# Optimization experiments

Measured on AMD Instinct MI355X. Metric: run time of the kernel, lower is better.

## Reference

```python
import jax, jax.numpy as jnp
import numpy as np

H = 256  # hidden_size
C = 512  # in_channels


def _gru_dir(x, w_ih, w_hh, b_ih, b_hh, reverse):
    # x: (B, T, Cin); w_ih: (3H, Cin); w_hh: (3H, H); gate order r,z,n (PyTorch)
    if reverse:
        x = x[:, ::-1, :]
    xp = jnp.einsum('btc,gc->btg', x, w_ih) + b_ih  # (B, T, 3H), batched GEMM
    h0 = jnp.zeros((x.shape[0], w_hh.shape[1]), x.dtype)

    def step(h, xp_t):  # xp_t: (B, 3H)
        gh = h @ w_hh.T + b_hh
        xr, xz, xn = jnp.split(xp_t, 3, axis=-1)
        hr, hz, hn = jnp.split(gh, 3, axis=-1)
        r = jax.nn.sigmoid(xr + hr)
        z = jax.nn.sigmoid(xz + hz)
        n = jnp.tanh(xn + r * hn)
        h_new = (1.0 - z) * n + z * h
        return h_new, h_new

    _, ys = jax.lax.scan(step, h0, jnp.swapaxes(xp, 0, 1))  # (T, B, H)
    ys = jnp.swapaxes(ys, 0, 1)  # (B, T, H)
    if reverse:
        ys = ys[:, ::-1, :]
    return ys


def _bigru_layer(x, wf, whf, bf, bhf, wr, whr, br, bhr):
    fwd = _gru_dir(x, wf, whf, bf, bhf, reverse=False)
    bwd = _gru_dir(x, wr, whr, br, bhr, reverse=True)
    return jnp.concatenate([fwd, bwd], axis=-1)  # (B, T, 2H)


def setup_inputs() -> dict:
    key = jax.random.key(0)
    ks = jax.random.split(key, 17)
    k = 1.0 / np.sqrt(H)  # PyTorch default init bound
    u = lambda kk, shp: jax.random.uniform(kk, shp, jnp.float32, -k, k)
    x = jax.random.normal(ks[0], (64, 512, 512, 1), jnp.float32)
    inp = {'x': x}
    # layer 0: input size C; layer 1: input size 2H
    sizes = {'l0': C, 'l1': 2 * H}
    i = 1
    for layer in ('l0', 'l1'):
        cin = sizes[layer]
        for d in ('f', 'r'):
            inp[f'w_ih_{layer}{d}'] = u(ks[i], (3 * H, cin)); i += 1
            inp[f'w_hh_{layer}{d}'] = u(ks[i], (3 * H, H)); i += 1
            inp[f'b_ih_{layer}{d}'] = u(ks[i], (3 * H,)); i += 1
            inp[f'b_hh_{layer}{d}'] = u(ks[i], (3 * H,)); i += 1
    return inp


def reference(x, w_ih_l0f, w_hh_l0f, b_ih_l0f, b_hh_l0f,
              w_ih_l0r, w_hh_l0r, b_ih_l0r, b_hh_l0r,
              w_ih_l1f, w_hh_l1f, b_ih_l1f, b_hh_l1f,
              w_ih_l1r, w_hh_l1r, b_ih_l1r, b_hh_l1r):
    b, c, w, h = x.shape
    seq = x.reshape(b, c, w * h).transpose(0, 2, 1)  # (B, T, C)
    y0 = _bigru_layer(seq, w_ih_l0f, w_hh_l0f, b_ih_l0f, b_hh_l0f,
                      w_ih_l0r, w_hh_l0r, b_ih_l0r, b_hh_l0r)
    y1 = _bigru_layer(y0, w_ih_l1f, w_hh_l1f, b_ih_l1f, b_hh_l1f,
                      w_ih_l1r, w_hh_l1r, b_ih_l1r, b_hh_l1r)
    return y1  # (B, T, 2H)
```

## Files before the change

### kernel.cpp

```cpp
#include <hip/hip_runtime.h>


typedef unsigned short u16;
typedef unsigned char u8;
typedef __attribute__((ext_vector_type(8))) short short8;
typedef __attribute__((ext_vector_type(4))) float f32x4;
typedef __attribute__((ext_vector_type(4))) int i32x4;

#define C1 (-1.4426950408889634f)
#define C2 (-2.8853900817779268f)
#define QS 258064.0f
#define C1S (C1 / QS)
#define C2S (C2 / QS)
#define MAGIC 12582912.0f

static __device__ __forceinline__ u16 f2bf(float x){
  union { float f; unsigned u; } v; v.f = x;
  unsigned r = v.u + 0x7fffu + ((v.u >> 16) & 1u);
  return (u16)(r >> 16);
}
static __device__ __forceinline__ float bf2f(u16 b){
  union { float f; unsigned u; } v; v.u = ((unsigned)b) << 16;
  return v.f;
}
static __device__ __forceinline__ unsigned cvt_pk_bf16(float lo, float hi){
  unsigned d;
  asm("v_cvt_pk_bf16_f32 %0, %1, %2" : "=v"(d) : "v"(lo), "v"(hi));
  return d;
}
static __device__ __forceinline__ unsigned q8(float x, float scale){
  union { float f; unsigned u; } v; v.f = fmaf(x, scale, MAGIC);
  return v.u & 0xffu;
}
#if __has_builtin(__builtin_amdgcn_exp2f)
#define EXP2(x) __builtin_amdgcn_exp2f(x)
#else
#define EXP2(x) exp2f(x)
#endif
#define RCP(x) __builtin_amdgcn_rcpf(x)

#define TT 512
#define BB 64
#define HH 256
#define GG 768
#define CC 512

#define HLB 320

__global__ __launch_bounds__(256) void k_transpose(const float* __restrict__ x,
                                                   u16* __restrict__ xT)
{
  __shared__ u16 tile[32][33];
  const int b  = blockIdx.z;
  const int c0 = blockIdx.y * 32, t0 = blockIdx.x * 32;
  const int tx = threadIdx.x & 31, ty = threadIdx.x >> 5;
  const float* xb = x + (size_t)b * CC * TT;
  #pragma unroll
  for (int i = 0; i < 4; ++i){
    int c = c0 + ty + i * 8;
    tile[ty + i * 8][tx] = f2bf(xb[(size_t)c * TT + t0 + tx]);
  }
  __syncthreads();
  const int bb2 = b >> 1, mrow = b & 1;
  #pragma unroll
  for (int i = 0; i < 4; ++i){
    int t = t0 + ty + i * 8;
    size_t rowp = ((size_t)bb2 * TT + t) * 2 + mrow;
    xT[rowp * CC + c0 + tx] = tile[tx][ty + i * 8];
  }
}

__global__ __launch_bounds__(256) void k_gemm(const u16* __restrict__ A,
    const float* __restrict__ wf, const float* __restrict__ wr,
    const float* __restrict__ bif, const float* __restrict__ bir,
    const float* __restrict__ bhf, const float* __restrict__ bhr,
    u16* __restrict__ xpA, u16* __restrict__ xpB)
{
  __shared__ u16 As[64][72];
  __shared__ u16 Bs[64][72];
  const int tid = threadIdx.x;
  const int n0  = blockIdx.x * 64;
  const int m0  = blockIdx.y * 64;
  const int dir = (n0 >= GG) ? 1 : 0;
  const int gb  = n0 - dir * GG;
  const float* W  = dir ? wr : wf;
  const float* BI = dir ? bir : bif;
  const float* BH = dir ? bhr : bhf;

  const int w = tid >> 6, l = tid & 63, q = l >> 4, r = l & 15;
  f32x4 acc[4] = {};

  for (int k0 = 0; k0 < CC; k0 += 64){
    #pragma unroll
    for (int i = 0; i < 2; ++i){
      int ch = tid + 256 * i;
      int row = ch >> 3, c8 = ch & 7;
      *(uint4*)&As[row][c8 * 8] =
          *(const uint4*)&A[(size_t)(m0 + row) * CC + k0 + c8 * 8];
    }
    #pragma unroll
    for (int i = 0; i < 4; ++i){
      int ch = tid + 256 * i;
      int row = ch >> 4, c4 = ch & 15;
      const float* s = &W[(size_t)(gb + row) * CC + k0 + c4 * 4];
      float4 fv = *(const float4*)s;
      unsigned p0 = (unsigned)f2bf(fv.x) | ((unsigned)f2bf(fv.y) << 16);
      unsigned p1 = (unsigned)f2bf(fv.z) | ((unsigned)f2bf(fv.w) << 16);
      *(uint2*)&Bs[row][c4 * 4] = make_uint2(p0, p1);
    }
    __syncthreads();
    #pragma unroll
    for (int kk = 0; kk < 2; ++kk){
      short8 a = *(const short8*)&As[w * 16 + r][kk * 32 + q * 8];
      #pragma unroll
      for (int nt = 0; nt < 4; ++nt){
        short8 b = *(const short8*)&Bs[nt * 16 + r][kk * 32 + q * 8];
        acc[nt] = __builtin_amdgcn_mfma_f32_16x16x32_bf16(a, b, acc[nt], 0, 0, 0);
      }
    }
    __syncthreads();
  }
  #pragma unroll
  for (int nt = 0; nt < 4; ++nt){
    const int g  = gb + nt * 16 + r;
    const int gi = g >> 8;
    const int c  = g & 255;
    const int wvl = c >> 5, cw = c & 31;
    const int ct = cw >> 4, rp = cw & 15;
    const float bias = (gi < 2) ? (BI[g] + BH[g]) : BI[g];
    const float sc   = (gi < 2) ? C1 : C2;
    #pragma unroll
    for (int j = 0; j < 4; ++j){
      const int row  = m0 + w * 16 + q * 4 + j;
      const int t    = (row >> 1) & 511;
      const int bb2  = row >> 10;
      const int mrow = row & 1;
      const int lane = wvl * 64 + (ct * 2 + mrow) * 16 + rp;
      const size_t base = ((size_t)(dir * 32 + bb2) * TT + t) * 512 + lane;
      const u16 v = f2bf(sc * (acc[nt][j] + bias));
      if (gi < 2) xpA[base * 2 + gi] = v;
      else        xpB[base]          = v;
    }
  }
}

template<int OUT_F32>
__global__ __launch_bounds__(512, 2) void k_rec(
    const u16* __restrict__ xpA, const u16* __restrict__ xpB,
    const float* __restrict__ whf, const float* __restrict__ whr,
    const float* __restrict__ bhf, const float* __restrict__ bhr,
    void* __restrict__ yout)
{
  __shared__ __align__(16) u8 hl[2][2][HLB];
  const int tid = threadIdx.x;
  const int d = blockIdx.x >> 5, bb2 = blockIdx.x & 31;
  const int wv = tid >> 6, l = tid & 63, q = l >> 4, r = l & 15;
  const int upper = (l >= 32);
  const int rodd  = q & 1;
  const int rl = l & 1;
  const float* WH = d ? whr : whf;
  const float* BH = d ? bhr : bhf;

  i32x4 Bf[3][2][4];
  #pragma unroll
  for (int gi = 0; gi < 3; ++gi)
    #pragma unroll
    for (int ct = 0; ct < 2; ++ct){
      int g = gi * HH + wv * 32 + ct * 16 + r;
      #pragma unroll
      for (int kk = 0; kk < 4; ++kk){
        const float* s = &WH[(size_t)g * HH + kk * 64 + q * 16];
        i32x4 bfv;
        #pragma unroll
        for (int c4 = 0; c4 < 4; ++c4){
          float4 fv = *(const float4*)(s + c4 * 4);
          unsigned b0 = q8(fv.x, 2032.0f);
          unsigned b1 = q8(fv.y, 2032.0f);
          unsigned b2 = q8(fv.z, 2032.0f);
          unsigned b3 = q8(fv.w, 2032.0f);
          bfv[c4] = (int)(b0 | (b1 << 8) | (b2 << 16) | (b3 << 24));
        }
        Bf[gi][ct][kk] = bfv;
      }
    }

  const int col = wv * 32 + (upper ? 16 : 0) + r;
  const float bnl = C2 * BH[2 * HH + col];
  float ho = 0.0f;

  for (int i = tid; i < 2 * 2 * HLB; i += 512) ((u8*)hl)[i] = 0;

  const int t0 = d ? (TT - 1) : 0;
  const int dstep = d ? -1 : 1;

  const size_t blk = (size_t)(d * 32 + bb2) * TT;
  const u16* pxA = xpA + ((blk + t0) * 512 + tid) * 2;
  const u16* pxB = xpB + ((blk + t0) * 512 + tid);
  const ptrdiff_t pxAs = (ptrdiff_t)dstep * 512 * 2;
  const ptrdiff_t pxBs = (ptrdiff_t)dstep * 512;

  struct XP { unsigned a; u16 b; };
  XP cxA, cxB;
  cxA.a = *(const unsigned*)pxA;  cxA.b = *pxB;
  pxA += pxAs; pxB += pxBs;

  u16*   py = nullptr;  float* pf = nullptr;
  if (OUT_F32){
    float* yf = (float*)yout;
    pf = yf + (((size_t)(bb2 * 2 + rodd) * TT + t0) * (2 * HH)) + (size_t)d * HH + col;
  } else {
    u16* yb = (u16*)yout;
    py = yb + (((size_t)bb2 * TT + t0) * 2 + rodd) * 512 + (size_t)d * HH + col;
  }
  const ptrdiff_t pys = (ptrdiff_t)dstep * 2 * 512;
  const ptrdiff_t pfs = (ptrdiff_t)dstep * 2 * HH;

  __syncthreads();

  auto step = [&](int s, int cur, XP* cxu, XP* cxl) {
    const int nxt = cur ^ 1;
    cxl->a = *(const unsigned*)pxA;
    cxl->b = *pxB;
    if (s < TT - 2){ pxA += pxAs; pxB += pxBs; }

    i32x4 acc[3][2] = {};
    #pragma unroll
    for (int kk = 0; kk < 4; ++kk){
      i32x4 af = *(const i32x4*)&hl[cur][rl][kk * 64 + q * 16];
      #pragma unroll
      for (int gi = 0; gi < 3; ++gi){
        acc[gi][0] = __builtin_amdgcn_mfma_i32_16x16x64_i8(af, Bf[gi][0][kk], acc[gi][0], 0, 0, 0);
        acc[gi][1] = __builtin_amdgcn_mfma_i32_16x16x64_i8(af, Bf[gi][1][kk], acc[gi][1], 0, 0, 0);
      }
    }
    int x00 = upper ? acc[0][1][0] : acc[0][0][0];
    int x01 = upper ? acc[0][1][1] : acc[0][0][1];
    int x10 = upper ? acc[1][1][0] : acc[1][0][0];
    int x11 = upper ? acc[1][1][1] : acc[1][0][1];
    int x20 = upper ? acc[2][1][0] : acc[2][0][0];
    int x21 = upper ? acc[2][1][1] : acc[2][0][1];
    float a0f = (float)(rodd ? x01 : x00);
    float a1f = (float)(rodd ? x11 : x10);
    float a2f = (float)(rodd ? x21 : x20);
    float xrp = bf2f((u16)(cxu->a & 0xffffu));
    float xzp = bf2f((u16)(cxu->a >> 16));
    float xnp = bf2f(cxu->b);
    float er = EXP2(fmaf(a0f, C1S, xrp));
    float ez = EXP2(fmaf(a1f, C1S, xzp));
    float sr = 1.0f + er, sz = 1.0f + ez;
    float R  = RCP(sr * sz);
    float rr = sz * R;
    float zz = sr * R;
    float inner = fmaf(a2f, C2S, bnl);
    float e2 = EXP2(fmaf(rr, inner, xnp));
    float nn = fmaf(2.0f, RCP(1.0f + e2), -1.0f);
    float hv = fmaf(zz, ho - nn, nn);
    ho = hv;
    hl[nxt][rodd][col] = (u8)q8(hv, 127.0f);
    if (OUT_F32){
      pf[0] = hv;
      pf += pfs;
    } else {
      py[0] = (u16)cvt_pk_bf16(hv, hv);
      py += pys;
    }
    asm volatile("s_waitcnt lgkmcnt(0)" ::: "memory");
    __builtin_amdgcn_s_barrier();
    asm volatile("" ::: "memory");
  };

  #pragma unroll 1
  for (int s = 0; s < TT; s += 2){
    step(s,     0, &cxA, &cxB);
    step(s + 1, 1, &cxB, &cxA);
  }
}

extern "C" void kernel_launch(void* const* d_in, const int* in_sizes, int n_in,
                              void* d_out, int out_size, void* d_ws, size_t ws_size,
                              hipStream_t stream)
{
  const float* x        = (const float*)d_in[0];
  const float* w_ih_l0f = (const float*)d_in[1];
  const float* w_hh_l0f = (const float*)d_in[2];
  const float* b_ih_l0f = (const float*)d_in[3];
  const float* b_hh_l0f = (const float*)d_in[4];
  const float* w_ih_l0r = (const float*)d_in[5];
  const float* w_hh_l0r = (const float*)d_in[6];
  const float* b_ih_l0r = (const float*)d_in[7];
  const float* b_hh_l0r = (const float*)d_in[8];
  const float* w_ih_l1f = (const float*)d_in[9];
  const float* w_hh_l1f = (const float*)d_in[10];
  const float* b_ih_l1f = (const float*)d_in[11];
  const float* b_hh_l1f = (const float*)d_in[12];
  const float* w_ih_l1r = (const float*)d_in[13];
  const float* w_hh_l1r = (const float*)d_in[14];
  const float* b_ih_l1r = (const float*)d_in[15];
  const float* b_hh_l1r = (const float*)d_in[16];

  u16* xT  = (u16*)d_ws;
  u16* xpA = xT  + (size_t)BB * TT * CC;
  u16* xpB = xpA + (size_t)64 * TT * 512 * 2;
  u16* y0  = xT;
  (void)in_sizes; (void)n_in; (void)out_size; (void)ws_size;

  k_transpose<<<dim3(TT / 32, CC / 32, BB), 256, 0, stream>>>(x, xT);

  k_gemm<<<dim3(2 * GG / 64, BB * TT / 64), 256, 0, stream>>>(
      xT, w_ih_l0f, w_ih_l0r, b_ih_l0f, b_ih_l0r, b_hh_l0f, b_hh_l0r, xpA, xpB);

  k_rec<0><<<dim3(64), 512, 0, stream>>>(xpA, xpB, w_hh_l0f, w_hh_l0r, b_hh_l0f, b_hh_l0r, (void*)y0);

  k_gemm<<<dim3(2 * GG / 64, BB * TT / 64), 256, 0, stream>>>(
      y0, w_ih_l1f, w_ih_l1r, b_ih_l1f, b_ih_l1r, b_hh_l1f, b_hh_l1r, xpA, xpB);

  k_rec<1><<<dim3(64), 512, 0, stream>>>(xpA, xpB, w_hh_l1f, w_hh_l1r, b_hh_l1f, b_hh_l1r, d_out);
}
```

Baseline: 942.1 us.

## Pre-convert input weights to bf16 and reorder recurrent MFMA chain

Adds a small kernel that converts the input-projection weights to bf16 once per layer, so the GEMM loads bf16 weight tiles directly instead of loading fp32 and converting in every block. In the recurrent step, the per-step MFMA loop is reordered so the r/z gate accumulators finish first. This lets their sigmoid math overlap with the n-gate MFMAs. The unconditional pointer advance drops a branch but reads one row past the end on the last step. The changes add an extra launch and workspace use in exchange for less redundant conversion work and a shorter critical path per timestep.

```diff
diff --git a/kernel.cpp b/kernel.cpp
--- a/kernel.cpp
+++ b/kernel.cpp
@@ -38,6 +38,7 @@
 #define EXP2(x) exp2f(x)
 #endif
 #define RCP(x) __builtin_amdgcn_rcpf(x)
+#define MFI8(a,b,c) __builtin_amdgcn_mfma_i32_16x16x64_i8((a),(b),(c),0,0,0)
 
 #define TT 512
 #define BB 64
@@ -46,6 +47,18 @@
 #define CC 512
 
 #define HLB 320
+
+__global__ __launch_bounds__(256) void k_wconv(const float* __restrict__ wf,
+    const float* __restrict__ wr, u16* __restrict__ Wb)
+{
+  const int idx = (blockIdx.x * 256 + threadIdx.x) * 4;
+  const int half = GG * CC;
+  const float* src = (idx < half) ? (wf + idx) : (wr + (idx - half));
+  float4 v = *(const float4*)src;
+  unsigned p0 = (unsigned)f2bf(v.x) | ((unsigned)f2bf(v.y) << 16);
+  unsigned p1 = (unsigned)f2bf(v.z) | ((unsigned)f2bf(v.w) << 16);
+  *(uint2*)&Wb[idx] = make_uint2(p0, p1);
+}
 
 __global__ __launch_bounds__(256) void k_transpose(const float* __restrict__ x,
                                                    u16* __restrict__ xT)
@@ -71,7 +84,7 @@
 }
 
 __global__ __launch_bounds__(256) void k_gemm(const u16* __restrict__ A,
-    const float* __restrict__ wf, const float* __restrict__ wr,
+    const u16* __restrict__ Wb,
     const float* __restrict__ bif, const float* __restrict__ bir,
     const float* __restrict__ bhf, const float* __restrict__ bhr,
     u16* __restrict__ xpA, u16* __restrict__ xpB)
@@ -83,7 +96,6 @@
   const int m0  = blockIdx.y * 64;
   const int dir = (n0 >= GG) ? 1 : 0;
   const int gb  = n0 - dir * GG;
-  const float* W  = dir ? wr : wf;
   const float* BI = dir ? bir : bif;
   const float* BH = dir ? bhr : bhf;
 
@@ -97,16 +109,8 @@
       int row = ch >> 3, c8 = ch & 7;
       *(uint4*)&As[row][c8 * 8] =
           *(const uint4*)&A[(size_t)(m0 + row) * CC + k0 + c8 * 8];
-    }
-    #pragma unroll
-    for (int i = 0; i < 4; ++i){
-      int ch = tid + 256 * i;
-      int row = ch >> 4, c4 = ch & 15;
-      const float* s = &W[(size_t)(gb + row) * CC + k0 + c4 * 4];
-      float4 fv = *(const float4*)s;
-      unsigned p0 = (unsigned)f2bf(fv.x) | ((unsigned)f2bf(fv.y) << 16);
-      unsigned p1 = (unsigned)f2bf(fv.z) | ((unsigned)f2bf(fv.w) << 16);
-      *(uint2*)&Bs[row][c4 * 4] = make_uint2(p0, p1);
+      *(uint4*)&Bs[row][c8 * 8] =
+          *(const uint4*)&Wb[(size_t)(n0 + row) * CC + k0 + c8 * 8];
     }
     __syncthreads();
     #pragma unroll
@@ -187,6 +191,7 @@
   const int col = wv * 32 + (upper ? 16 : 0) + r;
   const float bnl = C2 * BH[2 * HH + col];
   float ho = 0.0f;
+  const i32x4 ZACC = {};
 
   for (int i = tid; i < 2 * 2 * HLB; i += 512) ((u8*)hl)[i] = 0;
 
@@ -221,36 +226,47 @@
     const int nxt = cur ^ 1;
     cxl->a = *(const unsigned*)pxA;
     cxl->b = *pxB;
-    if (s < TT - 2){ pxA += pxAs; pxB += pxBs; }
-
-    i32x4 acc[3][2] = {};
-    #pragma unroll
-    for (int kk = 0; kk < 4; ++kk){
-      i32x4 af = *(const i32x4*)&hl[cur][rl][kk * 64 + q * 16];
-      #pragma unroll
-      for (int gi = 0; gi < 3; ++gi){
-        acc[gi][0] = __builtin_amdgcn_mfma_i32_16x16x64_i8(af, Bf[gi][0][kk], acc[gi][0], 0, 0, 0);
-        acc[gi][1] = __builtin_amdgcn_mfma_i32_16x16x64_i8(af, Bf[gi][1][kk], acc[gi][1], 0, 0, 0);
-      }
-    }
-    int x00 = upper ? acc[0][1][0] : acc[0][0][0];
-    int x01 = upper ? acc[0][1][1] : acc[0][0][1];
-    int x10 = upper ? acc[1][1][0] : acc[1][0][0];
-    int x11 = upper ? acc[1][1][1] : acc[1][0][1];
-    int x20 = upper ? acc[2][1][0] : acc[2][0][0];
-    int x21 = upper ? acc[2][1][1] : acc[2][0][1];
-    float a0f = (float)(rodd ? x01 : x00);
-    float a1f = (float)(rodd ? x11 : x10);
-    float a2f = (float)(rodd ? x21 : x20);
+    pxA += pxAs; pxB += pxBs;
+
+    i32x4 af0 = *(const i32x4*)&hl[cur][rl][0 * 64 + q * 16];
+    i32x4 af1 = *(const i32x4*)&hl[cur][rl][1 * 64 + q * 16];
+    i32x4 af2 = *(const i32x4*)&hl[cur][rl][2 * 64 + q * 16];
+    i32x4 af3 = *(const i32x4*)&hl[cur][rl][3 * 64 + q * 16];
+
+    i32x4 a00 = MFI8(af0, Bf[0][0][0], ZACC);
+    i32x4 a01 = MFI8(af0, Bf[0][1][0], ZACC);
+    i32x4 a10 = MFI8(af0, Bf[1][0][0], ZACC);
+    i32x4 a11 = MFI8(af0, Bf[1][1][0], ZACC);
+    a00 = MFI8(af1, Bf[0][0][1], a00);  a01 = MFI8(af1, Bf[0][1][1], a01);
+    a10 = MFI8(af1, Bf[1][0][1], a10);  a11 = MFI8(af1, Bf[1][1][1], a11);
+    a00 = MFI8(af2, Bf[0][0][2], a00);  a01 = MFI8(af2, Bf[0][1][2], a01);
+    a10 = MFI8(af2, Bf[1][0][2], a10);  a11 = MFI8(af2, Bf[1][1][2], a11);
+    a00 = MFI8(af3, Bf[0][0][3], a00);  a01 = MFI8(af3, Bf[0][1][3], a01);
+    a10 = MFI8(af3, Bf[1][0][3], a10);  a11 = MFI8(af3, Bf[1][1][3], a11);
+    i32x4 a20 = MFI8(af0, Bf[2][0][0], ZACC);
+    i32x4 a21 = MFI8(af0, Bf[2][1][0], ZACC);
+    a20 = MFI8(af1, Bf[2][0][1], a20);  a21 = MFI8(af1, Bf[2][1][1], a21);
+    a20 = MFI8(af2, Bf[2][0][2], a20);  a21 = MFI8(af2, Bf[2][1][2], a21);
+    a20 = MFI8(af3, Bf[2][0][3], a20);  a21 = MFI8(af3, Bf[2][1][3], a21);
+
+    int e00 = upper ? a01[0] : a00[0];
+    int e01 = upper ? a01[1] : a00[1];
+    int e10 = upper ? a11[0] : a10[0];
+    int e11 = upper ? a11[1] : a10[1];
+    float a0f = (float)(rodd ? e01 : e00);
+    float a1f = (float)(rodd ? e11 : e10);
     float xrp = bf2f((u16)(cxu->a & 0xffffu));
     float xzp = bf2f((u16)(cxu->a >> 16));
-    float xnp = bf2f(cxu->b);
     float er = EXP2(fmaf(a0f, C1S, xrp));
     float ez = EXP2(fmaf(a1f, C1S, xzp));
     float sr = 1.0f + er, sz = 1.0f + ez;
     float R  = RCP(sr * sz);
     float rr = sz * R;
     float zz = sr * R;
+    int e20 = upper ? a21[0] : a20[0];
+    int e21 = upper ? a21[1] : a20[1];
+    float a2f = (float)(rodd ? e21 : e20);
+    float xnp = bf2f(cxu->b);
     float inner = fmaf(a2f, C2S, bnl);
     float e2 = EXP2(fmaf(rr, inner, xnp));
     float nn = fmaf(2.0f, RCP(1.0f + e2), -1.0f);
@@ -301,18 +317,21 @@
   u16* xT  = (u16*)d_ws;
   u16* xpA = xT  + (size_t)BB * TT * CC;
   u16* xpB = xpA + (size_t)64 * TT * 512 * 2;
+  u16* Wb  = xpB + (size_t)64 * TT * 512;
   u16* y0  = xT;
   (void)in_sizes; (void)n_in; (void)out_size; (void)ws_size;
 
   k_transpose<<<dim3(TT / 32, CC / 32, BB), 256, 0, stream>>>(x, xT);
 
+  k_wconv<<<dim3(2 * GG * CC / 1024), 256, 0, stream>>>(w_ih_l0f, w_ih_l0r, Wb);
   k_gemm<<<dim3(2 * GG / 64, BB * TT / 64), 256, 0, stream>>>(
-      xT, w_ih_l0f, w_ih_l0r, b_ih_l0f, b_ih_l0r, b_hh_l0f, b_hh_l0r, xpA, xpB);
+      xT, Wb, b_ih_l0f, b_ih_l0r, b_hh_l0f, b_hh_l0r, xpA, xpB);
 
   k_rec<0><<<dim3(64), 512, 0, stream>>>(xpA, xpB, w_hh_l0f, w_hh_l0r, b_hh_l0f, b_hh_l0r, (void*)y0);
 
+  k_wconv<<<dim3(2 * GG * CC / 1024), 256, 0, stream>>>(w_ih_l1f, w_ih_l1r, Wb);
   k_gemm<<<dim3(2 * GG / 64, BB * TT / 64), 256, 0, stream>>>(
-      y0, w_ih_l1f, w_ih_l1r, b_ih_l1f, b_ih_l1r, b_hh_l1f, b_hh_l1r, xpA, xpB);
+      y0, Wb, b_ih_l1f, b_ih_l1r, b_hh_l1f, b_hh_l1r, xpA, xpB);
 
   k_rec<1><<<dim3(64), 512, 0, stream>>>(xpA, xpB, w_hh_l1f, w_hh_l1r, b_hh_l1f, b_hh_l1r, d_out);
 }
```

Result: faster. 849.2 us (-9.9%).
